# Kernel optimization log

Hardware: AMD Instinct MI355X
Metric: run time of the kernel (lower is better)

Reference implementation:

```python
import jax, jax.numpy as jnp
import numpy as np

B, A = 8192, 16
HID, NK, NQ, NV = 256, 32, 32, 128
IN_DIM, CUR_HID, CUR_OUT, N_ACT = 512, 512, 128, 64
EXT_LAMBD, INT_LAMBD = 1.0, 0.5


def setup_inputs() -> dict:
    key = jax.random.key(0)
    ks = jax.random.split(key, 16)
    def w(k, i, o):
        return jax.random.normal(k, (i, o), jnp.float32) / np.sqrt(i)
    return {
        'x': jax.random.normal(ks[0], (B * A, IN_DIM), jnp.float32),
        'hidden': jax.random.normal(ks[1], (B, A, HID), jnp.float32),
        'Wk': w(ks[2], HID, NK), 'bk': jnp.zeros((NK,), jnp.float32),
        'Wv': w(ks[3], HID, NV), 'bv': jnp.zeros((NV,), jnp.float32),
        'Wq': w(ks[4], HID, NQ), 'bq': jnp.zeros((NQ,), jnp.float32),
        'Wa': w(ks[5], NQ + NK * A, A), 'ba': jnp.zeros((A,), jnp.float32),
        'Wt1': w(ks[6], IN_DIM, CUR_HID), 'bt1': jnp.zeros((CUR_HID,), jnp.float32),
        'Wt2': w(ks[7], CUR_HID, CUR_OUT), 'bt2': jnp.zeros((CUR_OUT,), jnp.float32),
        'Wp1': w(ks[8], IN_DIM, CUR_HID), 'bp1': jnp.zeros((CUR_HID,), jnp.float32),
        'Wp2': w(ks[9], CUR_HID, CUR_HID), 'bp2': jnp.zeros((CUR_HID,), jnp.float32),
        'Wp3': w(ks[10], CUR_HID, CUR_OUT), 'bp3': jnp.zeros((CUR_OUT,), jnp.float32),
        'Wc': w(ks[11], NV + HID, HID), 'bc': jnp.zeros((HID,), jnp.float32),
        'W2': w(ks[12], HID, N_ACT), 'b2': jnp.zeros((N_ACT,), jnp.float32),
    }


def _aggregate(x, hidden, Wk, bk, Wv, bv, Wq, bq, Wa, ba, Wt1, bt1, Wt2, bt2,
               Wp1, bp1, Wp2, bp2, Wp3, bp3, Wc, bc, W2, b2):
    # communicate(): per-agent key / value / query projections
    key_ = hidden @ Wk + bk          # [B, A, NK]
    value = hidden @ Wv + bv         # [B, A, NV]
    query = hidden @ Wq + bq         # [B, A, NQ]
    # torch.cat([key[:, i, :] for i in range(A)], -1) == reshape; repeat == broadcast
    flat_key = key_.reshape(B, A * NK)
    qk = jnp.concatenate(
        [query, jnp.broadcast_to(flat_key[:, None, :], (B, A, A * NK))], axis=-1)
    attn_weights = jax.nn.softmax(qk @ Wa + ba, axis=-1)   # [B, A, A]
    # intrinsic-motivation predictors (dropout p=0.5 in eval mode -> identity)
    tar = jax.nn.relu(x @ Wt1 + bt1) @ Wt2 + bt2           # [B*A, CUR_OUT]
    pred = jax.nn.relu(x @ Wp1 + bp1)
    pred = jax.nn.relu(pred @ Wp2 + bp2)
    pred = pred @ Wp3 + bp3
    int_imp = jnp.mean((tar - pred) ** 2, axis=-1).reshape(B, A)
    int_imp = jax.nn.softmax(int_imp, axis=-1)             # [B, A]
    # view(B,A,1).repeat(1,1,A).permute(0,2,1): out[b,i,j] = int_imp[b,j]
    int_mat = jnp.broadcast_to(int_imp[:, None, :], (B, A, A))
    attn = EXT_LAMBD * attn_weights + INT_LAMBD * jax.lax.stop_gradient(int_mat)
    applied = jnp.einsum('bij,bjv->biv', attn, value)      # [B, A, NV]
    comb = jax.nn.relu(jnp.concatenate([applied, hidden], axis=-1) @ Wc + bc)
    return comb @ W2 + b2                                  # [B, A, N_ACT]


def reference(x, hidden, Wk, bk, Wv, bv, Wq, bq, Wa, ba, Wt1, bt1, Wt2, bt2,
              Wp1, bp1, Wp2, bp2, Wp3, bp3, Wc, bc, W2, b2):
    return _aggregate(x, hidden, Wk, bk, Wv, bv, Wq, bq, Wa, ba, Wt1, bt1,
                      Wt2, bt2, Wp1, bp1, Wp2, bp2, Wp3, bp3, Wc, bc, W2, b2)
```

## Files before the change

### kernel.cpp

```cpp
#include <hip/hip_runtime.h>
#include <cstddef>
#include <cstdint>

typedef unsigned short ushort_t;
typedef __attribute__((ext_vector_type(4))) float f32x4;
typedef __attribute__((ext_vector_type(8))) short bf16x8;

#define BB   8192
#define AA   16
#define BA   131072

__device__ __forceinline__ float bf2f(ushort_t u) {
    union { float f; uint32_t i; } v; v.i = ((uint32_t)u) << 16; return v.f;
}
__device__ __forceinline__ ushort_t f2bf(float f) {
    union { float f; uint32_t i; } v; v.f = f;
    uint32_t r = v.i + 0x7fffu + ((v.i >> 16) & 1u);
    return (ushort_t)(r >> 16);
}
__device__ __forceinline__ void gload_lds16(const void* g, void* l) {
    __builtin_amdgcn_global_load_lds(
        (const __attribute__((address_space(1))) uint32_t*)g,
        (__attribute__((address_space(3))) uint32_t*)l, 16, 0, 0);
}

template<bool RELU>
__global__ __launch_bounds__(512, 2)
void gemm8p(const ushort_t* __restrict__ A, int lda,
            const ushort_t* __restrict__ A2, int lda2, int ksplit,
            const ushort_t* __restrict__ Bt,
            const float* __restrict__ bias,
            ushort_t* __restrict__ C, int ldc, int K, int lgx, int rpx)
{
    __shared__ ushort_t lds[65536];

    const int tid  = threadIdx.x;
    const int w    = tid >> 6;
    const int lane = tid & 63;
    const int wm   = w >> 2;
    const int wn   = w & 3;
    const int fr   = lane & 15;
    const int fq   = lane >> 4;

    const int bid  = blockIdx.x;
    const int xcd  = bid & 7;
    const int slot = bid >> 3;
    const int x    = slot & ((1 << lgx) - 1);
    const int y    = xcd * rpx + (slot >> lgx);
    const size_t brow = (size_t)y * 256;
    const int    bcol = x * 256;

    const int NT = K >> 6;
    const int NI = NT >> 1;

    const int srl = tid >> 3;
    const int spg = tid & 7;

    f32x4 acc[8][4];
#pragma unroll
    for (int m = 0; m < 8; ++m)
#pragma unroll
        for (int n = 0; n < 4; ++n) acc[m][n] = (f32x4){0.f, 0.f, 0.f, 0.f};

    auto stageA = [&](int T, int s, int bi) {
        const int k0  = T << 6;
        const int row = (srl < 32) ? s * 32 + srl : 128 + s * 32 + (srl - 32);
        const int col = ((spg ^ (row & 7)) << 3);
        const ushort_t* src;
        if (k0 >= ksplit) src = A2 + (brow + row) * (size_t)lda2 + (k0 - ksplit) + col;
        else              src = A  + (brow + row) * (size_t)lda  + k0 + col;
        gload_lds16(src, &lds[(bi << 15) + row * 64 + spg * 8]);
    };
    auto stageB = [&](int T, int c, int bi) {
        const int k0  = T << 6;
        const int row = c * 64 + srl;
        const int col = ((spg ^ (row & 7)) << 3);
        gload_lds16(Bt + (size_t)(bcol + row) * K + k0 + col,
                    &lds[(bi << 15) + 16384 + row * 64 + spg * 8]);
    };

    stageA(0, 0, 0); stageB(0, 0, 0);
    stageA(0, 1, 0); stageB(0, 1, 0);
    stageA(0, 2, 0); stageB(0, 2, 0);
    stageA(0, 3, 0); stageB(0, 3, 0);
    stageA(1, 0, 1); stageB(1, 0, 1);
    stageA(1, 1, 1); stageB(1, 1, 1);
    stageA(1, 2, 1); stageB(1, 2, 1);

    bf16x8 breg[4][2];

    for (int i = 0; i < NI; ++i) {
        const bool more = (i + 1 < NI);
#pragma unroll
        for (int h = 0; h < 2; ++h) {
            const int bufA = h << 15;
            const int bufB = (h << 15) + 16384;
#pragma unroll
            for (int q = 0; q < 4; ++q) {
                if (q == 0) {
                    if (h == 0 || more) asm volatile("s_waitcnt vmcnt(6)" ::: "memory");
                    else                asm volatile("s_waitcnt vmcnt(0)" ::: "memory");
                    __builtin_amdgcn_sched_barrier(0);
                    __builtin_amdgcn_s_barrier();
#pragma unroll
                    for (int n = 0; n < 4; ++n)
#pragma unroll
                        for (int kk = 0; kk < 2; ++kk) {
                            const int row = wn * 64 + n * 16 + fr;
                            const int gp  = ((kk * 4 + fq) ^ (row & 7)) << 3;
                            breg[n][kk] = *(const bf16x8*)&lds[bufB + row * 64 + gp];
                        }
                }
                bf16x8 areg[2][2];
#pragma unroll
                for (int j = 0; j < 2; ++j)
#pragma unroll
                    for (int kk = 0; kk < 2; ++kk) {
                        const int row = wm * 128 + (2 * q + j) * 16 + fr;
                        const int gp  = ((kk * 4 + fq) ^ (row & 7)) << 3;
                        areg[j][kk] = *(const bf16x8*)&lds[bufA + row * 64 + gp];
                    }
                if (h == 0) {
                    if (q == 0)      { stageA(2*i+1, 3, 1); stageB(2*i+1, 3, 1); }
                    else if (more)   { stageA(2*i+2, q-1, 0); stageB(2*i+2, q-1, 0); }
                } else {
                    if (q == 0) { if (more) { stageA(2*i+2, 3, 0); stageB(2*i+2, 3, 0); } }
                    else        { if (more) { stageA(2*i+3, q-1, 1); stageB(2*i+3, q-1, 1); } }
                }
                __builtin_amdgcn_s_barrier();
                __builtin_amdgcn_s_setprio(1);
#pragma unroll
                for (int j = 0; j < 2; ++j)
#pragma unroll
                    for (int n = 0; n < 4; ++n)
#pragma unroll
                        for (int kk = 0; kk < 2; ++kk)
                            acc[2*q+j][n] = __builtin_amdgcn_mfma_f32_16x16x32_bf16(
                                areg[j][kk], breg[n][kk], acc[2*q+j][n], 0, 0, 0);
                __builtin_amdgcn_s_setprio(0);
                __builtin_amdgcn_s_barrier();
            }
        }
    }

#pragma unroll
    for (int m = 0; m < 8; ++m) {
        const size_t rowb = brow + wm * 128 + m * 16 + fq * 4;
#pragma unroll
        for (int n = 0; n < 4; ++n) {
            const int col = bcol + wn * 64 + n * 16 + fr;
            const float bv = bias[col];
#pragma unroll
            for (int r = 0; r < 4; ++r) {
                float v = acc[m][n][r] + bv;
                if (RELU) v = fmaxf(v, 0.f);
                C[(rowb + r) * (size_t)ldc + col] = f2bf(v);
            }
        }
    }
}

template<bool OBF16, bool RELU, bool MSE>
__global__ __launch_bounds__(256)
void gemm_mfma(const ushort_t* __restrict__ A, int lda,
               const ushort_t* __restrict__ A2, int lda2, int ksplit,
               const ushort_t* __restrict__ Bt,
               const float* __restrict__ bias,
               void* __restrict__ C, int ldc, int N, int K, int lgx,
               float* __restrict__ iimp_out)
{
    __shared__ ushort_t As[2][128 * 64];
    __shared__ ushort_t Bs[2][128 * 64];

    const int tid  = threadIdx.x;
    const int w    = tid >> 6;
    const int lane = tid & 63;
    const int wm   = w >> 1;
    const int wn   = w & 1;

    const int bid  = blockIdx.x;
    const int xcd  = bid & 7;
    const int slot = bid >> 3;
    const int x    = slot & ((1 << lgx) - 1);
    const int y    = xcd * 128 + (slot >> lgx);
    const size_t brow = (size_t)y * 128;
    const int    bcol = x * 128;

    const int fr   = lane & 15;
    const int fq   = lane >> 4;
    const int srow = lane >> 3;
    const int scol = (lane & 7) << 3;

    f32x4 acc[4][4];
#pragma unroll
    for (int i = 0; i < 4; ++i)
#pragma unroll
        for (int j = 0; j < 4; ++j) acc[i][j] = (f32x4){0.f, 0.f, 0.f, 0.f};

    const int NT = K >> 6;

    auto stage = [&](int buf, int k0) {
#pragma unroll
        for (int i = 0; i < 4; ++i) {
            const int c = (w << 2) + i;
            const int r = (c << 3) + srow;
            const ushort_t* asrc;
            if (k0 >= ksplit)
                asrc = A2 + (brow + r) * (size_t)lda2 + (k0 - ksplit) + scol;
            else
                asrc = A  + (brow + r) * (size_t)lda  + k0 + scol;
            gload_lds16(asrc, &As[buf][(c << 9) + lane * 8]);
            gload_lds16(Bt + (size_t)(bcol + r) * K + k0 + scol,
                        &Bs[buf][(c << 9) + lane * 8]);
        }
    };

    stage(0, 0);
    __syncthreads();

    for (int t = 0; t < NT; ++t) {
        const int cur = t & 1;
        if (t + 1 < NT) stage(cur ^ 1, (t + 1) << 6);
#pragma unroll
        for (int kk = 0; kk < 2; ++kk) {
            bf16x8 a[4], b[4];
#pragma unroll
            for (int f = 0; f < 4; ++f) {
                a[f] = *(const bf16x8*)&As[cur][(wm * 64 + f * 16 + fr) * 64 + kk * 32 + fq * 8];
                b[f] = *(const bf16x8*)&Bs[cur][(wn * 64 + f * 16 + fr) * 64 + kk * 32 + fq * 8];
            }
#pragma unroll
            for (int fm = 0; fm < 4; ++fm)
#pragma unroll
                for (int fn = 0; fn < 4; ++fn)
                    acc[fm][fn] = __builtin_amdgcn_mfma_f32_16x16x32_bf16(
                        a[fm], b[fn], acc[fm][fn], 0, 0, 0);
        }
        __syncthreads();
    }

    if (MSE) {
        float* rowsq = (float*)As;
        if (tid < 128) rowsq[tid] = 0.f;
        __syncthreads();
#pragma unroll
        for (int fm = 0; fm < 4; ++fm) {
#pragma unroll
            for (int r = 0; r < 4; ++r) {
                float s = 0.f;
#pragma unroll
                for (int fn = 0; fn < 4; ++fn) {
                    const int col = wn * 64 + fn * 16 + fr;
                    const float v = acc[fm][fn][r] + bias[col];
                    s += v * v;
                }
                s += __shfl_xor(s, 1);
                s += __shfl_xor(s, 2);
                s += __shfl_xor(s, 4);
                s += __shfl_xor(s, 8);
                if (fr == 0)
                    atomicAdd(&rowsq[wm * 64 + fm * 16 + fq * 4 + r], s);
            }
        }
        __syncthreads();
        if (tid < 8) {
            const int rb = tid * 16;
            float mv[16], mx = -1e30f;
#pragma unroll
            for (int a = 0; a < 16; ++a) {
                mv[a] = rowsq[rb + a] * (1.f / 128.f);
                mx = fmaxf(mx, mv[a]);
            }
            float e[16], den = 0.f;
#pragma unroll
            for (int a = 0; a < 16; ++a) { e[a] = __expf(mv[a] - mx); den += e[a]; }
            const float inv = 1.f / den;
            const size_t b = brow / 16 + tid;
#pragma unroll
            for (int a = 0; a < 16; ++a) iimp_out[b * 16 + a] = e[a] * inv;
        }
        return;
    }

#pragma unroll
    for (int fm = 0; fm < 4; ++fm) {
        const size_t rowb = brow + wm * 64 + fm * 16 + fq * 4;
#pragma unroll
        for (int fn = 0; fn < 4; ++fn) {
            const int col = bcol + wn * 64 + fn * 16 + fr;
            if (col < N) {
                const float bv = bias[col];
#pragma unroll
                for (int r = 0; r < 4; ++r) {
                    float v = acc[fm][fn][r] + bv;
                    if (RELU) v = fmaxf(v, 0.f);
                    const size_t idx = (rowb + r) * (size_t)ldc + col;
                    if (OBF16) ((ushort_t*)C)[idx] = f2bf(v);
                    else       ((float*)C)[idx]    = v;
                }
            }
        }
    }
}

__global__ __launch_bounds__(256)
void transpose_w(const float* __restrict__ W, ushort_t* __restrict__ Wt,
                 int K, int N, int Npad)
{
    int idx = blockIdx.x * 256 + threadIdx.x;
    if (idx >= Npad * K) return;
    int n = idx / K, k = idx - n * K;
    float v = (n < N) ? W[(size_t)k * N + n] : 0.f;
    Wt[idx] = f2bf(v);
}

__global__ __launch_bounds__(256)
void transpose_wk(const float* __restrict__ W, ushort_t* __restrict__ Wt,
                  int Ksrc, int N, int ldk, int kOff, float sign)
{
    int idx = blockIdx.x * 256 + threadIdx.x;
    if (idx >= N * Ksrc) return;
    int n = idx / Ksrc, k = idx - n * Ksrc;
    Wt[(size_t)n * ldk + kOff + k] = f2bf(sign * W[(size_t)k * N + n]);
}

__global__ __launch_bounds__(256)
void conv_f32_bf16(const float* __restrict__ src, ushort_t* __restrict__ dst)
{
    size_t q = (size_t)blockIdx.x * 256 + threadIdx.x;
    float4 v = ((const float4*)src)[q];
    ushort_t* d = dst + q * 4;
    d[0] = f2bf(v.x); d[1] = f2bf(v.y); d[2] = f2bf(v.z); d[3] = f2bf(v.w);
}

__global__ void pack_cat2(const float* __restrict__ a, const float* __restrict__ b,
                          float* __restrict__ o)
{
    int j = blockIdx.x * 256 + threadIdx.x;
    if (j < 512) o[j] = a[j];
    else if (j < 1024) o[j] = b[j - 512];
}

__global__ void pack_bias(const float* __restrict__ bk, const float* __restrict__ bq,
                          const float* __restrict__ bv, float* __restrict__ pb)
{
    int j = threadIdx.x;
    float v = 0.f;
    if      (j < 32)  v = bk[j];
    else if (j < 64)  v = bq[j - 32];
    else if (j < 192) v = bv[j - 64];
    pb[j] = v;
}

__global__ void make_cbias(const float* __restrict__ bt2, const float* __restrict__ bp3,
                           float* __restrict__ cb)
{
    int j = threadIdx.x;
    cb[j] = bt2[j] - bp3[j];
}

__global__ __launch_bounds__(256)
void attn_apply(const ushort_t* __restrict__ kvq, const float* __restrict__ Wa,
                const float* __restrict__ ba, const float* __restrict__ iimp,
                ushort_t* __restrict__ applied)
{
    const int b = blockIdx.x, t = threadIdx.x;
    __shared__ float klds[512], qlds[512];
    __shared__ ushort_t vlds[2048];
    __shared__ float part[16][17];
    __shared__ float kp[16];
    __shared__ float attn[16][17];

    for (int i = t; i < 512; i += 256) {
        int a = i >> 5, c = i & 31;
        const size_t base = ((size_t)b * AA + a) * 192;
        klds[i] = bf2f(kvq[base + c]);
        qlds[i] = bf2f(kvq[base + 32 + c]);
    }
    for (int i = t; i < 2048; i += 256) {
        int j = i >> 7, v = i & 127;
        vlds[i] = kvq[((size_t)b * AA + j) * 192 + 64 + v];
    }
    __syncthreads();

    {
        int j = t & 15, seg = t >> 4;
        float s = 0.f;
        for (int c = seg * 32; c < seg * 32 + 32; ++c)
            s += klds[c] * Wa[(32 + c) * 16 + j];
        part[j][seg] = s;
    }
    __syncthreads();
    if (t < 16) {
        float s = 0.f;
#pragma unroll
        for (int seg = 0; seg < 16; ++seg) s += part[t][seg];
        kp[t] = s;
    }
    __syncthreads();

    {
        int i = t >> 4, j = t & 15;
        float s = 0.f;
#pragma unroll
        for (int q = 0; q < 32; ++q) s += qlds[i * 32 + q] * Wa[q * 16 + j];
        attn[i][j] = s + kp[j] + ba[j];
    }
    __syncthreads();
    if (t < 16) {
        float mx = -1e30f;
#pragma unroll
        for (int j = 0; j < 16; ++j) mx = fmaxf(mx, attn[t][j]);
        float e[16], den = 0.f;
#pragma unroll
        for (int j = 0; j < 16; ++j) { e[j] = __expf(attn[t][j] - mx); den += e[j]; }
        float inv = 1.f / den;
#pragma unroll
        for (int j = 0; j < 16; ++j)
            attn[t][j] = e[j] * inv + 0.5f * iimp[b * 16 + j];
    }
    __syncthreads();

    for (int o = t; o < 2048; o += 256) {
        int i = o >> 7, v = o & 127;
        float s = 0.f;
#pragma unroll
        for (int j = 0; j < 16; ++j) s += attn[i][j] * bf2f(vlds[j * 128 + v]);
        applied[((size_t)b * AA + i) * 128 + v] = f2bf(s);
    }
}

extern "C" void kernel_launch(void* const* d_in, const int* in_sizes, int n_in,
                              void* d_out, int out_size, void* d_ws, size_t ws_size,
                              hipStream_t stream)
{
    const float* x      = (const float*)d_in[0];
    const float* hidden = (const float*)d_in[1];
    const float* Wk  = (const float*)d_in[2];
    const float* bk  = (const float*)d_in[3];
    const float* Wv  = (const float*)d_in[4];
    const float* bv  = (const float*)d_in[5];
    const float* Wq  = (const float*)d_in[6];
    const float* bq  = (const float*)d_in[7];
    const float* Wa  = (const float*)d_in[8];
    const float* ba  = (const float*)d_in[9];
    const float* Wt1 = (const float*)d_in[10];
    const float* bt1 = (const float*)d_in[11];
    const float* Wt2 = (const float*)d_in[12];
    const float* bt2 = (const float*)d_in[13];
    const float* Wp1 = (const float*)d_in[14];
    const float* bp1 = (const float*)d_in[15];
    const float* Wp2 = (const float*)d_in[16];
    const float* bp2 = (const float*)d_in[17];
    const float* Wp3 = (const float*)d_in[18];
    const float* bp3 = (const float*)d_in[19];
    const float* Wc  = (const float*)d_in[20];
    const float* bc  = (const float*)d_in[21];
    const float* W2  = (const float*)d_in[22];
    const float* b2  = (const float*)d_in[23];

    float*    out = (float*)d_out;
    ushort_t* ws  = (ushort_t*)d_ws;

    ushort_t* xb  = ws;
    ushort_t* ht2 = xb + (size_t)BA * 512;
    ushort_t* hp2 = ht2 + (size_t)BA * 1024;
    ushort_t* WT  = hp2 + (size_t)BA * 512;
    ushort_t* kvq     = xb;
    ushort_t* hiddenb = hp2;
    ushort_t* applied = ht2;
    ushort_t* comb    = ht2 + (size_t)BA * 128;

    ushort_t* Bg1  = WT;
    ushort_t* Wp2t = Bg1  + 1024 * 512;
    ushort_t* Dt   = Wp2t + 512 * 512;
    ushort_t* Wkvq = Dt   + 128 * 1024;
    ushort_t* Wct  = Wkvq + 256 * 256;
    ushort_t* W2t  = Wct  + 256 * 384;
    float* g1bias = (float*)(W2t + 128 * 256);
    float* pbias  = g1bias + 1024;
    float* cbias  = pbias + 256;
    float* iimp   = cbias + 128;

    const dim3 blk(256);
    const int BIG = 1 << 30;

    transpose_w<<<1024, blk, 0, stream>>>(Wt1, Bg1,             512, 512, 512);
    transpose_w<<<1024, blk, 0, stream>>>(Wp1, Bg1 + 512 * 512, 512, 512, 512);
    transpose_w<<<1024, blk, 0, stream>>>(Wp2, Wp2t, 512, 512, 512);
    transpose_wk<<<256, blk, 0, stream>>>(Wt2, Dt, 512, 128, 1024, 0,    1.f);
    transpose_wk<<<256, blk, 0, stream>>>(Wp3, Dt, 512, 128, 1024, 512, -1.f);
    transpose_w<<<32,  blk, 0, stream>>>(Wk, Wkvq + 0 * 256,   256, 32, 32);
    transpose_w<<<32,  blk, 0, stream>>>(Wq, Wkvq + 32 * 256,  256, 32, 32);
    transpose_w<<<128, blk, 0, stream>>>(Wv, Wkvq + 64 * 256,  256, 128, 128);
    transpose_w<<<64,  blk, 0, stream>>>(Wk, Wkvq + 192 * 256, 256, 0, 64);
    transpose_w<<<384, blk, 0, stream>>>(Wc, Wct, 384, 256, 256);
    transpose_w<<<128, blk, 0, stream>>>(W2, W2t, 256, 64, 128);
    pack_cat2<<<4, 256, 0, stream>>>(bt1, bp1, g1bias);
    pack_bias<<<1, 256, 0, stream>>>(bk, bq, bv, pbias);
    make_cbias<<<1, 128, 0, stream>>>(bt2, bp3, cbias);

    conv_f32_bf16<<<65536, blk, 0, stream>>>(x, xb);
    gemm8p<true><<<2048, 512, 0, stream>>>(
        xb, 512, xb, 512, BIG, Bg1, g1bias, ht2, 1024, 512, 2, 64);
    gemm8p<true><<<1024, 512, 0, stream>>>(
        ht2 + 512, 1024, ht2 + 512, 1024, BIG, Wp2t, bp2, hp2, 512, 512, 1, 64);
    gemm_mfma<true, false, true><<<1024, blk, 0, stream>>>(
        ht2, 1024, hp2, 512, 512, Dt, cbias, nullptr, 128, 128, 1024, 0, iimp);

    conv_f32_bf16<<<32768, blk, 0, stream>>>(hidden, hiddenb);
    gemm_mfma<true, false, false><<<2048, blk, 0, stream>>>(
        hiddenb, 256, hiddenb, 256, BIG, Wkvq, pbias, kvq, 192, 192, 256, 1, nullptr);
    attn_apply<<<BB, blk, 0, stream>>>(kvq, Wa, ba, iimp, applied);

    gemm8p<true><<<512, 512, 0, stream>>>(
        applied, 128, hiddenb, 256, 128, Wct, bc, comb, 256, 384, 0, 64);
    gemm_mfma<false, false, false><<<1024, blk, 0, stream>>>(
        comb, 256, comb, 256, BIG, W2t, b2, out, 64, 64, 256, 0, nullptr);
}
```

Before: 633.0 us.

## Fuse final W2 projection into combine GEMM epilogue via LDS

The combine GEMM (concat of applied and hidden times Wc, ReLU) now keeps its 256x256 bf16 tile in swizzled LDS. It then runs the final W2 projection with MFMA in the epilogue and writes fp32 outputs directly. This removes the intermediate comb buffer write and read and one kernel launch. It also adds an explicit lgkmcnt wait before the barrier in the pipelined main loop, which affects every gemm8p call. The cost is higher register use from the W2 fragments held in registers and a longer epilogue.

```diff
diff --git a/kernel.cpp b/kernel.cpp
--- a/kernel.cpp
+++ b/kernel.cpp
@@ -24,13 +24,14 @@
         (__attribute__((address_space(3))) uint32_t*)l, 16, 0, 0);
 }
 
-template<bool RELU>
+template<bool RELU, bool FUSE_OUT>
 __global__ __launch_bounds__(512, 2)
 void gemm8p(const ushort_t* __restrict__ A, int lda,
             const ushort_t* __restrict__ A2, int lda2, int ksplit,
             const ushort_t* __restrict__ Bt,
             const float* __restrict__ bias,
-            ushort_t* __restrict__ C, int ldc, int K, int lgx, int rpx)
+            ushort_t* __restrict__ C, int ldc, int K, int lgx, int rpx,
+            const ushort_t* __restrict__ W2t, const float* __restrict__ b2)
 {
     __shared__ ushort_t lds[65536];
 
@@ -127,6 +128,7 @@
                     if (q == 0) { if (more) { stageA(2*i+2, 3, 0); stageB(2*i+2, 3, 0); } }
                     else        { if (more) { stageA(2*i+3, q-1, 1); stageB(2*i+3, q-1, 1); } }
                 }
+                if (q == 0) asm volatile("s_waitcnt lgkmcnt(8)" ::: "memory");
                 __builtin_amdgcn_s_barrier();
                 __builtin_amdgcn_s_setprio(1);
 #pragma unroll
@@ -143,18 +145,75 @@
         }
     }
 
-#pragma unroll
-    for (int m = 0; m < 8; ++m) {
-        const size_t rowb = brow + wm * 128 + m * 16 + fq * 4;
-#pragma unroll
-        for (int n = 0; n < 4; ++n) {
-            const int col = bcol + wn * 64 + n * 16 + fr;
-            const float bv = bias[col];
-#pragma unroll
-            for (int r = 0; r < 4; ++r) {
-                float v = acc[m][n][r] + bv;
-                if (RELU) v = fmaxf(v, 0.f);
-                C[(rowb + r) * (size_t)ldc + col] = f2bf(v);
+    if (!FUSE_OUT) {
+#pragma unroll
+        for (int m = 0; m < 8; ++m) {
+            const size_t rowb = brow + wm * 128 + m * 16 + fq * 4;
+#pragma unroll
+            for (int n = 0; n < 4; ++n) {
+                const int col = bcol + wn * 64 + n * 16 + fr;
+                const float bv = bias[col];
+#pragma unroll
+                for (int r = 0; r < 4; ++r) {
+                    float v = acc[m][n][r] + bv;
+                    if (RELU) v = fmaxf(v, 0.f);
+                    C[(rowb + r) * (size_t)ldc + col] = f2bf(v);
+                }
+            }
+        }
+    } else {
+#pragma unroll
+        for (int m = 0; m < 8; ++m) {
+            const int row = wm * 128 + m * 16 + fq * 4;
+#pragma unroll
+            for (int n = 0; n < 4; ++n) {
+                const int col = wn * 64 + n * 16 + fr;
+                const float bv = bias[col];
+#pragma unroll
+                for (int r = 0; r < 4; ++r) {
+                    const float v = fmaxf(acc[m][n][r] + bv, 0.f);
+                    const int rr = row + r;
+                    const int g  = (col >> 3) ^ (rr & 7);
+                    lds[rr * 256 + g * 8 + (col & 7)] = f2bf(v);
+                }
+            }
+        }
+        bf16x8 w2f[4][8];
+#pragma unroll
+        for (int n2 = 0; n2 < 4; ++n2)
+#pragma unroll
+            for (int kk = 0; kk < 8; ++kk)
+                w2f[n2][kk] = *(const bf16x8*)&W2t[(n2 * 16 + fr) * 256 + kk * 32 + fq * 8];
+        __syncthreads();
+        f32x4 acc2[2][4];
+#pragma unroll
+        for (int m2 = 0; m2 < 2; ++m2)
+#pragma unroll
+            for (int n2 = 0; n2 < 4; ++n2) acc2[m2][n2] = (f32x4){0.f, 0.f, 0.f, 0.f};
+#pragma unroll
+        for (int kk = 0; kk < 8; ++kk) {
+#pragma unroll
+            for (int m2 = 0; m2 < 2; ++m2) {
+                const int row = w * 32 + m2 * 16 + fr;
+                const int g   = (kk * 4 + fq) ^ (row & 7);
+                const bf16x8 af = *(const bf16x8*)&lds[row * 256 + g * 8];
+#pragma unroll
+                for (int n2 = 0; n2 < 4; ++n2)
+                    acc2[m2][n2] = __builtin_amdgcn_mfma_f32_16x16x32_bf16(
+                        af, w2f[n2][kk], acc2[m2][n2], 0, 0, 0);
+            }
+        }
+        float* outp = (float*)C;
+#pragma unroll
+        for (int m2 = 0; m2 < 2; ++m2) {
+            const size_t rowb = brow + w * 32 + m2 * 16 + fq * 4;
+#pragma unroll
+            for (int n2 = 0; n2 < 4; ++n2) {
+                const int col = n2 * 16 + fr;
+                const float bv = b2[col];
+#pragma unroll
+                for (int r = 0; r < 4; ++r)
+                    outp[(rowb + r) * 64 + col] = acc2[m2][n2][r] + bv;
             }
         }
     }
@@ -469,7 +528,6 @@
     ushort_t* kvq     = xb;
     ushort_t* hiddenb = hp2;
     ushort_t* applied = ht2;
-    ushort_t* comb    = ht2 + (size_t)BA * 128;
 
     ushort_t* Bg1  = WT;
     ushort_t* Wp2t = Bg1  + 1024 * 512;
@@ -501,10 +559,10 @@
     make_cbias<<<1, 128, 0, stream>>>(bt2, bp3, cbias);
 
     conv_f32_bf16<<<65536, blk, 0, stream>>>(x, xb);
-    gemm8p<true><<<2048, 512, 0, stream>>>(
-        xb, 512, xb, 512, BIG, Bg1, g1bias, ht2, 1024, 512, 2, 64);
-    gemm8p<true><<<1024, 512, 0, stream>>>(
-        ht2 + 512, 1024, ht2 + 512, 1024, BIG, Wp2t, bp2, hp2, 512, 512, 1, 64);
+    gemm8p<true, false><<<2048, 512, 0, stream>>>(
+        xb, 512, xb, 512, BIG, Bg1, g1bias, ht2, 1024, 512, 2, 64, nullptr, nullptr);
+    gemm8p<true, false><<<1024, 512, 0, stream>>>(
+        ht2 + 512, 1024, ht2 + 512, 1024, BIG, Wp2t, bp2, hp2, 512, 512, 1, 64, nullptr, nullptr);
     gemm_mfma<true, false, true><<<1024, blk, 0, stream>>>(
         ht2, 1024, hp2, 512, 512, Dt, cbias, nullptr, 128, 128, 1024, 0, iimp);
 
@@ -513,8 +571,6 @@
         hiddenb, 256, hiddenb, 256, BIG, Wkvq, pbias, kvq, 192, 192, 256, 1, nullptr);
     attn_apply<<<BB, blk, 0, stream>>>(kvq, Wa, ba, iimp, applied);
 
-    gemm8p<true><<<512, 512, 0, stream>>>(
-        applied, 128, hiddenb, 256, 128, Wct, bc, comb, 256, 384, 0, 64);
-    gemm_mfma<false, false, false><<<1024, blk, 0, stream>>>(
-        comb, 256, comb, 256, BIG, W2t, b2, out, 64, 64, 256, 0, nullptr);
-}
+    gemm8p<true, true><<<512, 512, 0, stream>>>(
+        applied, 128, hiddenb, 256, 128, Wct, bc, (ushort_t*)out, 64, 384, 0, 64, W2t, b2);
+}
```

New measurement: 616.7 us. 1.03x faster.
